# Optimization experiments

Hardware: AMD Instinct MI355X
Metric: run time of the kernel (lower is better)

The kernel has to match this reference:

```python
import jax, jax.numpy as jnp
import numpy as np

M, N = 4096, 4096

def _make_expk(n):
    k = np.arange(n, dtype=np.float64) * np.pi / (2.0 * n)
    return jnp.asarray(np.stack([np.cos(k), np.sin(k)], axis=-1), dtype=jnp.float32)

def setup_inputs() -> dict:
    key = jax.random.key(0)
    x = jax.random.normal(key, (M, N), dtype=jnp.float32)
    return {"x": x, "expkM": _make_expk(M), "expkN": _make_expk(N)}

def _idct_last(X, expk):
    """1D IDCT (inverse of unnormalized DCT-II) along last axis via Makhoul's
    N-point FFT trick. expk[k] = (cos, sin) of pi*k/(2N), i.e. e^{j pi k/(2N)}."""
    n = X.shape[-1]
    Xv = X * 0.5
    # V[k] = (Xv[k] - j*Xv[n-k]) * e^{j pi k/(2n)}, with imag part 0 at k=0
    tail = -jnp.flip(Xv, axis=-1)[..., :-1]
    Vi = jnp.concatenate([jnp.zeros_like(Xv[..., :1]), tail], axis=-1)
    W = expk[:, 0] + 1j * expk[:, 1]
    V = (Xv + 1j * Vi) * W
    v = jnp.fft.ifft(V, axis=-1).real.astype(X.dtype)
    # de-interleave: out[2m] = v[m], out[2m+1] = v[n-1-m]
    out = jnp.zeros_like(X)
    out = out.at[..., 0::2].set(v[..., : n - n // 2])
    out = out.at[..., 1::2].set(jnp.flip(v, axis=-1)[..., : n // 2])
    return out

def reference(x, expkM, expkN):
    # separable 2D IDCT: last axis (N) then first axis (M)
    y = _idct_last(x, expkN)
    y = _idct_last(y.T, expkM).T
    return y
```

## Files before the change

kernel.cpp:

```cpp
#include <hip/hip_runtime.h>
#include <math.h>


#define TT 256

constexpr float W64R[32] = {
    1.0f, 0.995184726672197f, 0.980785280403230f, 0.956940335732209f,
    0.923879532511287f, 0.881921264348355f, 0.831469612302545f, 0.773010453362737f,
    0.707106781186548f, 0.634393284163645f, 0.555570233019602f, 0.471396736825998f,
    0.382683432365090f, 0.290284677254462f, 0.195090322016128f, 0.0980171403295606f,
    0.0f, -0.0980171403295606f, -0.195090322016128f, -0.290284677254462f,
    -0.382683432365090f, -0.471396736825998f, -0.555570233019602f, -0.634393284163645f,
    -0.707106781186548f, -0.773010453362737f, -0.831469612302545f, -0.881921264348355f,
    -0.923879532511287f, -0.956940335732209f, -0.980785280403230f, -0.995184726672197f};
constexpr float W64I[32] = {
    0.0f, 0.0980171403295606f, 0.195090322016128f, 0.290284677254462f,
    0.382683432365090f, 0.471396736825998f, 0.555570233019602f, 0.634393284163645f,
    0.707106781186548f, 0.773010453362737f, 0.831469612302545f, 0.881921264348355f,
    0.923879532511287f, 0.956940335732209f, 0.980785280403230f, 0.995184726672197f,
    1.0f, 0.995184726672197f, 0.980785280403230f, 0.956940335732209f,
    0.923879532511287f, 0.881921264348355f, 0.831469612302545f, 0.773010453362737f,
    0.707106781186548f, 0.634393284163645f, 0.555570233019602f, 0.471396736825998f,
    0.382683432365090f, 0.290284677254462f, 0.195090322016128f, 0.0980171403295606f};

__device__ __forceinline__ constexpr int brev(int x, int bits) {
    int r = 0;
    for (int i = 0; i < bits; ++i) { r = (r << 1) | (x & 1); x >>= 1; }
    return r;
}

template <int NP>
__device__ __forceinline__ void fft_dif(float2* a) {
#pragma unroll
    for (int h = NP / 2; h >= 1; h >>= 1) {
#pragma unroll
        for (int b = 0; b < NP; b += 2 * h) {
#pragma unroll
            for (int k = 0; k < h; ++k) {
                float2 u = a[b + k], v = a[b + k + h];
                float dx = u.x - v.x, dy = u.y - v.y;
                a[b + k] = make_float2(u.x + v.x, u.y + v.y);
                float wr = W64R[k * (32 / h)], wi = W64I[k * (32 / h)];
                a[b + k + h] = make_float2(dx * wr - dy * wi, dx * wi + dy * wr);
            }
        }
    }
}

__global__ void tw_init_kernel(float2* __restrict__ tw2048,
                               float2* __restrict__ c1, float2* __restrict__ c2,
                               float2* __restrict__ c3, float2* __restrict__ c4) {
    int t = threadIdx.x;
    const double s = 0.5 / 4096.0;
    for (int i = 0; i < 8; ++i) {
        int k = t + 256 * i;
        double aw = M_PI * (double)k / 2048.0;
        double wr = cos(aw), wi = sin(aw);
        double a1 = M_PI * (double)k / 8192.0;
        double e1r = cos(a1), e1i = sin(a1);
        double a2 = M_PI * (double)(k + 2048) / 8192.0;
        double e2r = cos(a2), e2i = sin(a2);
        double Ar = s * ((1.0 - wi) * e1r - wr * e1i);
        double Ai = s * ((1.0 - wi) * e1i + wr * e1r);
        double Br = (k == 0) ? 0.0 : Ai;
        double Bi = (k == 0) ? 0.0 : -Ar;
        double Cr = s * ((1.0 + wi) * e2r + wr * e2i);
        double Ci = s * ((1.0 + wi) * e2i - wr * e2r);
        c1[k] = make_float2((float)Ar, (float)Ai);
        c2[k] = make_float2((float)Br, (float)Bi);
        c3[k] = make_float2((float)Cr, (float)Ci);
        c4[k] = make_float2((float)Ci, (float)-Cr);
        double at = M_PI * (double)k / 1024.0;
        tw2048[k] = make_float2((float)cos(at), (float)sin(at));
    }
}

__global__ __launch_bounds__(TT) void col_a_kernel(
    const float* __restrict__ x,
    const float2* __restrict__ c1, const float2* __restrict__ c2,
    const float2* __restrict__ c3, const float2* __restrict__ c4,
    const float2* __restrict__ tw2048, float2* __restrict__ T1) {
    int c = blockIdx.x * 64 + threadIdx.x;
    int k1 = blockIdx.y * 4 + threadIdx.y;
    float2 f[32];
#pragma unroll
    for (int k2 = 0; k2 < 32; ++k2) {
        int k = k1 + 64 * k2;
        float xa = x[(size_t)k * 4096 + c];
        float xb = x[(size_t)((4096 - k) & 4095) * 4096 + c];
        float xc = x[(size_t)(2048 + k) * 4096 + c];
        float xd = x[(size_t)(2048 - k) * 4096 + c];
        float2 A = c1[k], B = c2[k], C = c3[k], D = c4[k];
        f[k2].x = A.x * xa + B.x * xb + C.x * xc + D.x * xd;
        f[k2].y = A.y * xa + B.y * xb + C.y * xc + D.y * xd;
    }
    fft_dif<32>(f);
#pragma unroll
    for (int j = 0; j < 32; ++j) {
        int n2 = brev(j, 5);
        float2 w = tw2048[k1 * n2];
        float2 v = f[j];
        float2 o = make_float2(v.x * w.x - v.y * w.y, v.x * w.y + v.y * w.x);
        T1[(size_t)(k1 * 32 + n2) * 4096 + c] = o;
    }
}

__global__ __launch_bounds__(TT) void col_b_kernel(
    const float2* __restrict__ T1, float* __restrict__ out) {
    int c = blockIdx.x * 64 + threadIdx.x;
    int n2 = blockIdx.y * 4 + threadIdx.y;
    float2 f[64];
#pragma unroll
    for (int k1 = 0; k1 < 64; ++k1)
        f[k1] = T1[(size_t)(k1 * 32 + n2) * 4096 + c];
    fft_dif<64>(f);
#pragma unroll
    for (int j = 0; j < 64; ++j) {
        int n1 = brev(j, 6);
        int m = 32 * n1 + n2;
        int r0 = (n1 < 32) ? (4 * m) : (8191 - 4 * m);
        int r1 = (n1 < 32) ? (4 * m + 2) : (8189 - 4 * m);
        out[(size_t)r0 * 4096 + c] = f[j].x;
        out[(size_t)r1 * 4096 + c] = f[j].y;
    }
}

#define C_SQ2 0.70710678118654752440f
__device__ __forceinline__ void radix8(const float* ar, const float* ai,
                                       float* tr, float* ti) {
    float s04r = ar[0] + ar[4], s04i = ai[0] + ai[4];
    float d04r = ar[0] - ar[4], d04i = ai[0] - ai[4];
    float s26r = ar[2] + ar[6], s26i = ai[2] + ai[6];
    float d26r = ar[2] - ar[6], d26i = ai[2] - ai[6];
    float E0r = s04r + s26r, E0i = s04i + s26i;
    float E1r = d04r - d26i, E1i = d04i + d26r;
    float E2r = s04r - s26r, E2i = s04i - s26i;
    float E3r = d04r + d26i, E3i = d04i - d26r;
    float s15r = ar[1] + ar[5], s15i = ai[1] + ai[5];
    float d15r = ar[1] - ar[5], d15i = ai[1] - ai[5];
    float s37r = ar[3] + ar[7], s37i = ai[3] + ai[7];
    float d37r = ar[3] - ar[7], d37i = ai[3] - ai[7];
    float O0r = s15r + s37r, O0i = s15i + s37i;
    float O1r = d15r - d37i, O1i = d15i + d37r;
    float O2r = s15r - s37r, O2i = s15i - s37i;
    float O3r = d15r + d37i, O3i = d15i - d37r;
    float W1r = C_SQ2 * (O1r - O1i), W1i = C_SQ2 * (O1r + O1i);
    float W2r = -O2i, W2i = O2r;
    float W3r = -C_SQ2 * (O3r + O3i), W3i = C_SQ2 * (O3r - O3i);
    tr[0] = E0r + O0r; ti[0] = E0i + O0i;
    tr[4] = E0r - O0r; ti[4] = E0i - O0i;
    tr[1] = E1r + W1r; ti[1] = E1i + W1i;
    tr[5] = E1r - W1r; ti[5] = E1i - W1i;
    tr[2] = E2r + W2r; ti[2] = E2i + W2i;
    tr[6] = E2r - W2r; ti[6] = E2i - W2i;
    tr[3] = E3r + W3r; ti[3] = E3i + W3i;
    tr[7] = E3r - W3r; ti[7] = E3i - W3i;
}

__global__ __launch_bounds__(TT) void idct_rows_kernel(
    const float2* __restrict__ c1, const float2* __restrict__ c2,
    const float2* __restrict__ c3, const float2* __restrict__ c4,
    const float2* __restrict__ tw2048, float* __restrict__ io) {
    __shared__ float b0r[2112], b0i[2112], b1r[2176], b1i[2176];
    const int t = threadIdx.x;
    float* __restrict__ xr = io + (size_t)blockIdx.x * 4096;

    float zr[8], zi[8], tr[8], ti[8];
#pragma unroll
    for (int p = 0; p < 8; ++p) {
        int k = t + 256 * p;
        float xa = xr[k];
        float xb = xr[(4096 - k) & 4095];
        float xc = xr[2048 + k];
        float xd = xr[2048 - k];
        float2 A = c1[k], B = c2[k], C = c3[k], D = c4[k];
        zr[p] = A.x * xa + B.x * xb + C.x * xc + D.x * xd;
        zi[p] = A.y * xa + B.y * xb + C.y * xc + D.y * xd;
    }
    radix8(zr, zi, tr, ti);
    {
        int baseA = 8 * t + (t >> 2);
        b0r[baseA] = tr[0]; b0i[baseA] = ti[0];
#pragma unroll
        for (int q = 1; q < 8; ++q) {
            float2 w = tw2048[(t * q) & 2047];
            b0r[baseA + q] = w.x * tr[q] - w.y * ti[q];
            b0i[baseA + q] = w.x * ti[q] + w.y * tr[q];
        }
    }
    __syncthreads();
    {
        float ar[8], ai[8];
        int rb = t + (t >> 5);
#pragma unroll
        for (int p = 0; p < 8; ++p) { ar[p] = b0r[rb + 264 * p]; ai[p] = b0i[rb + 264 * p]; }
        radix8(ar, ai, tr, ti);
        int j = t >> 3, k = t & 7, wj = 8 * j;
        int baseB = 68 * j + k;
        b1r[baseB] = tr[0]; b1i[baseB] = ti[0];
#pragma unroll
        for (int q = 1; q < 8; ++q) {
            int off = baseB + 8 * q + (q >> 1);
            float2 w = tw2048[(wj * q) & 2047];
            b1r[off] = w.x * tr[q] - w.y * ti[q];
            b1i[off] = w.x * ti[q] + w.y * tr[q];
        }
    }
    __syncthreads();
    {
        float ar[8], ai[8];
        int rb = t + (t >> 4);
#pragma unroll
        for (int p = 0; p < 8; ++p) { ar[p] = b1r[rb + 272 * p]; ai[p] = b1i[rb + 272 * p]; }
        radix8(ar, ai, tr, ti);
        int j = t >> 6, wj = 64 * j, k = t & 63;
        int baseC = 528 * j + k + (k >> 5);
        b0r[baseC] = tr[0]; b0i[baseC] = ti[0];
#pragma unroll
        for (int q = 1; q < 8; ++q) {
            int off = baseC + 66 * q;
            float2 w = tw2048[(wj * q) & 2047];
            b0r[off] = w.x * tr[q] - w.y * ti[q];
            b0i[off] = w.x * ti[q] + w.y * tr[q];
        }
    }
    __syncthreads();
#pragma unroll
    for (int u = 0; u < 2; ++u) {
        int b = t + 256 * u;
        int rb = b + (b >> 5);
        int wb = b + (b >> 4);
        float a0r = b0r[rb], a0i = b0i[rb];
        float a1r = b0r[rb + 528], a1i = b0i[rb + 528];
        float a2r = b0r[rb + 1056], a2i = b0i[rb + 1056];
        float a3r = b0r[rb + 1584], a3i = b0i[rb + 1584];
        float s02r = a0r + a2r, s02i = a0i + a2i;
        float d02r = a0r - a2r, d02i = a0i - a2i;
        float s13r = a1r + a3r, s13i = a1i + a3i;
        float d13r = a1r - a3r, d13i = a1i - a3i;
        b1r[wb] = s02r + s13r;          b1i[wb] = s02i + s13i;
        b1r[wb + 544] = d02r - d13i;    b1i[wb + 544] = d02i + d13r;
        b1r[wb + 1088] = s02r - s13r;   b1i[wb + 1088] = s02i - s13i;
        b1r[wb + 1632] = d02r + d13i;   b1i[wb + 1632] = d02i - d13r;
    }
    __syncthreads();
#pragma unroll
    for (int i = 0; i < 16; ++i) {
        int q = t + 256 * i;
        int vidx = (q & 1) ? (4095 - ((q - 1) >> 1)) : (q >> 1);
        int l = vidx >> 1;
        int m_ = l + (l >> 4);
        float val = (vidx & 1) ? b1i[m_] : b1r[m_];
        xr[q] = val;
    }
}

extern "C" void kernel_launch(void* const* d_in, const int* in_sizes, int n_in,
                              void* d_out, int out_size, void* d_ws, size_t ws_size,
                              hipStream_t stream) {
    const float* x = (const float*)d_in[0];
    float* out = (float*)d_out;

    float2* tw2048 = (float2*)d_ws;
    float2* c1 = (float2*)((char*)d_ws + 1 * 16384);
    float2* c2 = (float2*)((char*)d_ws + 2 * 16384);
    float2* c3 = (float2*)((char*)d_ws + 3 * 16384);
    float2* c4 = (float2*)((char*)d_ws + 4 * 16384);
    float2* T1 = (float2*)((char*)d_ws + (1 << 20));

    tw_init_kernel<<<1, TT, 0, stream>>>(tw2048, c1, c2, c3, c4);
    col_a_kernel<<<dim3(64, 16), dim3(64, 4), 0, stream>>>(x, c1, c2, c3, c4, tw2048, T1);
    col_b_kernel<<<dim3(64, 8), dim3(64, 4), 0, stream>>>(T1, out);
    idct_rows_kernel<<<4096, TT, 0, stream>>>(c1, c2, c3, c4, tw2048, out);
}
```

Before: 203.7 us.

## Vectorize global memory accesses across IDCT kernels and parallelize twiddle init

Column pass A now has each thread process two adjacent columns, using float2 loads and float4 stores. The FFT is templated so it can run on split real/imag arrays. Column pass B stages its scattered row outputs through shared memory so they can be written as coalesced float4 rows. The row kernel stages each input row in LDS with float4 loads and writes output as float4, and twiddle init runs on 8 blocks instead of one. This targets uncoalesced or scalar global traffic and the serial init cost, at the price of more registers (64 float2 in column A), extra LDS use and extra barriers.

```diff
diff --git a/kernel.cpp b/kernel.cpp
--- a/kernel.cpp
+++ b/kernel.cpp
@@ -29,99 +29,131 @@
     return r;
 }
 
-template <int NP>
-__device__ __forceinline__ void fft_dif(float2* a) {
+__device__ __forceinline__ float vadd(float a, float b) { return a + b; }
+__device__ __forceinline__ float vsub(float a, float b) { return a - b; }
+__device__ __forceinline__ float vmul(float a, float s) { return a * s; }
+__device__ __forceinline__ float2 vadd(float2 a, float2 b) { return make_float2(a.x + b.x, a.y + b.y); }
+__device__ __forceinline__ float2 vsub(float2 a, float2 b) { return make_float2(a.x - b.x, a.y - b.y); }
+__device__ __forceinline__ float2 vmul(float2 a, float s) { return make_float2(a.x * s, a.y * s); }
+
+template <int NP, typename V>
+__device__ __forceinline__ void fft_dif(V* re, V* im) {
 #pragma unroll
     for (int h = NP / 2; h >= 1; h >>= 1) {
 #pragma unroll
         for (int b = 0; b < NP; b += 2 * h) {
 #pragma unroll
             for (int k = 0; k < h; ++k) {
-                float2 u = a[b + k], v = a[b + k + h];
-                float dx = u.x - v.x, dy = u.y - v.y;
-                a[b + k] = make_float2(u.x + v.x, u.y + v.y);
+                V ur = re[b + k], ui = im[b + k];
+                V vr = re[b + k + h], vi = im[b + k + h];
+                V dr = vsub(ur, vr), di = vsub(ui, vi);
+                re[b + k] = vadd(ur, vr);
+                im[b + k] = vadd(ui, vi);
                 float wr = W64R[k * (32 / h)], wi = W64I[k * (32 / h)];
-                a[b + k + h] = make_float2(dx * wr - dy * wi, dx * wi + dy * wr);
+                re[b + k + h] = vsub(vmul(dr, wr), vmul(di, wi));
+                im[b + k + h] = vadd(vmul(dr, wi), vmul(di, wr));
             }
         }
     }
 }
 
 __global__ void tw_init_kernel(float2* __restrict__ tw2048,
-                               float2* __restrict__ c1, float2* __restrict__ c2,
-                               float2* __restrict__ c3, float2* __restrict__ c4) {
-    int t = threadIdx.x;
+                               float2* __restrict__ ca, float2* __restrict__ cb,
+                               float2* __restrict__ cc, float2* __restrict__ cd) {
+    int k = blockIdx.x * TT + threadIdx.x;
     const double s = 0.5 / 4096.0;
-    for (int i = 0; i < 8; ++i) {
-        int k = t + 256 * i;
-        double aw = M_PI * (double)k / 2048.0;
-        double wr = cos(aw), wi = sin(aw);
-        double a1 = M_PI * (double)k / 8192.0;
-        double e1r = cos(a1), e1i = sin(a1);
-        double a2 = M_PI * (double)(k + 2048) / 8192.0;
-        double e2r = cos(a2), e2i = sin(a2);
-        double Ar = s * ((1.0 - wi) * e1r - wr * e1i);
-        double Ai = s * ((1.0 - wi) * e1i + wr * e1r);
-        double Br = (k == 0) ? 0.0 : Ai;
-        double Bi = (k == 0) ? 0.0 : -Ar;
-        double Cr = s * ((1.0 + wi) * e2r + wr * e2i);
-        double Ci = s * ((1.0 + wi) * e2i - wr * e2r);
-        c1[k] = make_float2((float)Ar, (float)Ai);
-        c2[k] = make_float2((float)Br, (float)Bi);
-        c3[k] = make_float2((float)Cr, (float)Ci);
-        c4[k] = make_float2((float)Ci, (float)-Cr);
-        double at = M_PI * (double)k / 1024.0;
-        tw2048[k] = make_float2((float)cos(at), (float)sin(at));
-    }
+    double aw = M_PI * (double)k / 2048.0;
+    double wr = cos(aw), wi = sin(aw);
+    double a1 = M_PI * (double)k / 8192.0;
+    double e1r = cos(a1), e1i = sin(a1);
+    double a2 = M_PI * (double)(k + 2048) / 8192.0;
+    double e2r = cos(a2), e2i = sin(a2);
+    double Ar = s * ((1.0 - wi) * e1r - wr * e1i);
+    double Ai = s * ((1.0 - wi) * e1i + wr * e1r);
+    double Br = (k == 0) ? 0.0 : Ai;
+    double Bi = (k == 0) ? 0.0 : -Ar;
+    double Cr = s * ((1.0 + wi) * e2r + wr * e2i);
+    double Ci = s * ((1.0 + wi) * e2i - wr * e2r);
+    ca[k] = make_float2((float)Ar, (float)Ai);
+    cb[k] = make_float2((float)Br, (float)Bi);
+    cc[k] = make_float2((float)Cr, (float)Ci);
+    cd[k] = make_float2((float)Ci, (float)-Cr);
+    double at = M_PI * (double)k / 1024.0;
+    tw2048[k] = make_float2((float)cos(at), (float)sin(at));
 }
 
 __global__ __launch_bounds__(TT) void col_a_kernel(
     const float* __restrict__ x,
-    const float2* __restrict__ c1, const float2* __restrict__ c2,
-    const float2* __restrict__ c3, const float2* __restrict__ c4,
+    const float2* __restrict__ ca, const float2* __restrict__ cb,
+    const float2* __restrict__ cc, const float2* __restrict__ cd,
     const float2* __restrict__ tw2048, float2* __restrict__ T1) {
-    int c = blockIdx.x * 64 + threadIdx.x;
+    int c2 = blockIdx.x * 64 + threadIdx.x;
     int k1 = blockIdx.y * 4 + threadIdx.y;
-    float2 f[32];
+    const float2* __restrict__ xv = (const float2*)x;
+    float2 fr[32], fi[32];
 #pragma unroll
     for (int k2 = 0; k2 < 32; ++k2) {
         int k = k1 + 64 * k2;
-        float xa = x[(size_t)k * 4096 + c];
-        float xb = x[(size_t)((4096 - k) & 4095) * 4096 + c];
-        float xc = x[(size_t)(2048 + k) * 4096 + c];
-        float xd = x[(size_t)(2048 - k) * 4096 + c];
-        float2 A = c1[k], B = c2[k], C = c3[k], D = c4[k];
-        f[k2].x = A.x * xa + B.x * xb + C.x * xc + D.x * xd;
-        f[k2].y = A.y * xa + B.y * xb + C.y * xc + D.y * xd;
-    }
-    fft_dif<32>(f);
+        float2 xa = xv[(size_t)k * 2048 + c2];
+        float2 xb = xv[(size_t)((4096 - k) & 4095) * 2048 + c2];
+        float2 xc = xv[(size_t)(2048 + k) * 2048 + c2];
+        float2 xd = xv[(size_t)(2048 - k) * 2048 + c2];
+        float2 A = ca[k], B = cb[k], C = cc[k], D = cd[k];
+        fr[k2] = make_float2(A.x * xa.x + B.x * xb.x + C.x * xc.x + D.x * xd.x,
+                             A.x * xa.y + B.x * xb.y + C.x * xc.y + D.x * xd.y);
+        fi[k2] = make_float2(A.y * xa.x + B.y * xb.x + C.y * xc.x + D.y * xd.x,
+                             A.y * xa.y + B.y * xb.y + C.y * xc.y + D.y * xd.y);
+    }
+    fft_dif<32, float2>(fr, fi);
 #pragma unroll
     for (int j = 0; j < 32; ++j) {
         int n2 = brev(j, 5);
         float2 w = tw2048[k1 * n2];
-        float2 v = f[j];
-        float2 o = make_float2(v.x * w.x - v.y * w.y, v.x * w.y + v.y * w.x);
-        T1[(size_t)(k1 * 32 + n2) * 4096 + c] = o;
+        float2 orr = vsub(vmul(fr[j], w.x), vmul(fi[j], w.y));
+        float2 oii = vadd(vmul(fr[j], w.y), vmul(fi[j], w.x));
+        float4 o = make_float4(orr.x, oii.x, orr.y, oii.y);
+        *(float4*)&T1[(size_t)(k1 * 32 + n2) * 4096 + 2 * c2] = o;
     }
 }
 
 __global__ __launch_bounds__(TT) void col_b_kernel(
     const float2* __restrict__ T1, float* __restrict__ out) {
-    int c = blockIdx.x * 64 + threadIdx.x;
-    int n2 = blockIdx.y * 4 + threadIdx.y;
-    float2 f[64];
-#pragma unroll
-    for (int k1 = 0; k1 < 64; ++k1)
-        f[k1] = T1[(size_t)(k1 * 32 + n2) * 4096 + c];
-    fft_dif<64>(f);
-#pragma unroll
-    for (int j = 0; j < 64; ++j) {
-        int n1 = brev(j, 6);
-        int m = 32 * n1 + n2;
-        int r0 = (n1 < 32) ? (4 * m) : (8191 - 4 * m);
-        int r1 = (n1 < 32) ? (4 * m + 2) : (8189 - 4 * m);
-        out[(size_t)r0 * 4096 + c] = f[j].x;
-        out[(size_t)r1 * 4096 + c] = f[j].y;
+    __shared__ float L[128 * 68];
+    int tx = threadIdx.x, ty = threadIdx.y;
+    int c = blockIdx.x * 64 + tx;
+    int n2 = blockIdx.y * 4 + ty;
+    float re[64], im[64];
+#pragma unroll
+    for (int k1 = 0; k1 < 64; ++k1) {
+        float2 v = T1[(size_t)(k1 * 32 + n2) * 4096 + c];
+        re[k1] = v.x; im[k1] = v.y;
+    }
+    fft_dif<64, float>(re, im);
+    int tlin = ty * 64 + tx;
+#pragma unroll
+    for (int g = 0; g < 4; ++g) {
+        if (ty == g) {
+#pragma unroll
+            for (int j = 0; j < 64; ++j) {
+                int n1 = brev(j, 6);
+                L[(2 * n1) * 68 + tx] = re[j];
+                L[(2 * n1 + 1) * 68 + tx] = im[j];
+            }
+        }
+        __syncthreads();
+        int n2g = blockIdx.y * 4 + g;
+#pragma unroll
+        for (int u = 0; u < 8; ++u) {
+            int idx = tlin + 256 * u;
+            int slot = idx >> 4, xp = idx & 15;
+            int n1 = slot >> 1;
+            int m = 32 * n1 + n2g;
+            int row = (n1 < 32) ? (4 * m + ((slot & 1) ? 2 : 0))
+                                : (((slot & 1) ? 8189 : 8191) - 4 * m);
+            float4 v = *(const float4*)&L[slot * 68 + 4 * xp];
+            *(float4*)&out[(size_t)row * 4096 + blockIdx.x * 64 + 4 * xp] = v;
+        }
+        __syncthreads();
     }
 }
 
@@ -158,22 +190,35 @@
 }
 
 __global__ __launch_bounds__(TT) void idct_rows_kernel(
-    const float2* __restrict__ c1, const float2* __restrict__ c2,
-    const float2* __restrict__ c3, const float2* __restrict__ c4,
+    const float2* __restrict__ ca, const float2* __restrict__ cb,
+    const float2* __restrict__ cc, const float2* __restrict__ cd,
     const float2* __restrict__ tw2048, float* __restrict__ io) {
-    __shared__ float b0r[2112], b0i[2112], b1r[2176], b1i[2176];
+    __shared__ float pool[8576];
+    float* b0r = pool;
+    float* b0i = pool + 2112;
+    float* b1r = pool + 4224;
+    float* b1i = pool + 6400;
+    float* stg = pool + 4224;
     const int t = threadIdx.x;
     float* __restrict__ xr = io + (size_t)blockIdx.x * 4096;
 
+#pragma unroll
+    for (int u = 0; u < 4; ++u) {
+        int idx = t + 256 * u;
+        float4 v = ((const float4*)xr)[idx];
+        *(float4*)&stg[4 * idx] = v;
+    }
+    __syncthreads();
+
     float zr[8], zi[8], tr[8], ti[8];
 #pragma unroll
     for (int p = 0; p < 8; ++p) {
         int k = t + 256 * p;
-        float xa = xr[k];
-        float xb = xr[(4096 - k) & 4095];
-        float xc = xr[2048 + k];
-        float xd = xr[2048 - k];
-        float2 A = c1[k], B = c2[k], C = c3[k], D = c4[k];
+        float xa = stg[k];
+        float xb = stg[(4096 - k) & 4095];
+        float xc = stg[2048 + k];
+        float xd = stg[2048 - k];
+        float2 A = ca[k], B = cb[k], C = cc[k], D = cd[k];
         zr[p] = A.x * xa + B.x * xb + C.x * xc + D.x * xd;
         zi[p] = A.y * xa + B.y * xb + C.y * xc + D.y * xd;
     }
@@ -245,13 +290,13 @@
     }
     __syncthreads();
 #pragma unroll
-    for (int i = 0; i < 16; ++i) {
-        int q = t + 256 * i;
-        int vidx = (q & 1) ? (4095 - ((q - 1) >> 1)) : (q >> 1);
-        int l = vidx >> 1;
-        int m_ = l + (l >> 4);
-        float val = (vidx & 1) ? b1i[m_] : b1r[m_];
-        xr[q] = val;
+    for (int i = 0; i < 4; ++i) {
+        int s = t + 256 * i;
+        int l2 = 2047 - s;
+        int ms = s + (s >> 4);
+        int ml = l2 + (l2 >> 4);
+        float4 o = make_float4(b1r[ms], b1i[ml], b1i[ms], b1r[ml]);
+        *(float4*)&xr[4 * s] = o;
     }
 }
 
@@ -262,14 +307,14 @@
     float* out = (float*)d_out;
 
     float2* tw2048 = (float2*)d_ws;
-    float2* c1 = (float2*)((char*)d_ws + 1 * 16384);
-    float2* c2 = (float2*)((char*)d_ws + 2 * 16384);
-    float2* c3 = (float2*)((char*)d_ws + 3 * 16384);
-    float2* c4 = (float2*)((char*)d_ws + 4 * 16384);
+    float2* ca = (float2*)((char*)d_ws + 1 * 16384);
+    float2* cb = (float2*)((char*)d_ws + 2 * 16384);
+    float2* cc = (float2*)((char*)d_ws + 3 * 16384);
+    float2* cd = (float2*)((char*)d_ws + 4 * 16384);
     float2* T1 = (float2*)((char*)d_ws + (1 << 20));
 
-    tw_init_kernel<<<1, TT, 0, stream>>>(tw2048, c1, c2, c3, c4);
-    col_a_kernel<<<dim3(64, 16), dim3(64, 4), 0, stream>>>(x, c1, c2, c3, c4, tw2048, T1);
+    tw_init_kernel<<<8, TT, 0, stream>>>(tw2048, ca, cb, cc, cd);
+    col_a_kernel<<<dim3(32, 16), dim3(64, 4), 0, stream>>>(x, ca, cb, cc, cd, tw2048, T1);
     col_b_kernel<<<dim3(64, 8), dim3(64, 4), 0, stream>>>(T1, out);
-    idct_rows_kernel<<<4096, TT, 0, stream>>>(c1, c2, c3, c4, tw2048, out);
-}
+    idct_rows_kernel<<<4096, TT, 0, stream>>>(ca, cb, cc, cd, tw2048, out);
+}
```

Result: faster. 199.6 us (-2.0%).
